# Performance work log

Hardware: AMD Instinct MI355X
Metric: run time of the kernel (lower is better)

Reference implementation:

```python
import jax, jax.numpy as jnp
import numpy as np

B = 4096
D = 1024
N = 9000000
TEMPERATURE = 0.1
GAMMA = 0.8
ALPHA = 0.5
EPS = 1e-14


def setup_inputs() -> dict:
    key = jax.random.key(0)
    k1, k2, k3, k4, k5 = jax.random.split(key, 5)
    zis = jax.random.normal(k1, (B, D), dtype=jnp.float32)
    zjs = jax.random.normal(k2, (B, D), dtype=jnp.float32)
    s_I = jax.random.uniform(k3, (N,), dtype=jnp.float32)
    s_T = jax.random.uniform(k4, (N,), dtype=jnp.float32)
    b_I = jnp.zeros((N,), dtype=jnp.float32)
    b_T = jnp.zeros((N,), dtype=jnp.float32)
    ids = jax.random.randint(k5, (B,), 0, N, dtype=jnp.int64 if jax.config.jax_enable_x64 else jnp.int32)
    return {"zis": zis, "zjs": zjs, "s_I": s_I, "s_T": s_T, "b_I": b_I, "b_T": b_T, "ids": ids}


def reference(zis, zjs, s_I, s_T, b_I, b_T, ids):
    sg = jax.lax.stop_gradient
    # L2 normalize embeddings (norm=True path)
    zis = zis / jnp.linalg.norm(zis, axis=1, keepdims=True)
    zjs = zjs / jnp.linalg.norm(zjs, axis=1, keepdims=True)
    sim = jnp.einsum('id,jd->ij', zis, zjs)            # [B, B]
    diag = jnp.diagonal(sim)                            # [B]
    image_diffs = sim - diag[:, None]
    text_diffs = sim - diag[None, :]
    # detached, temperature-scaled diffs (torch .clone().detach_())
    idd = sg(image_diffs) / TEMPERATURE
    tdd = sg(text_diffs) / TEMPERATURE
    # online max tracking (per-id running max b)
    old_b_I = b_I[ids]                                  # gather [B]
    new_b_I = jnp.maximum(idd.max(axis=1), old_b_I)
    old_b_T = b_T[ids]
    new_b_T = jnp.maximum(tdd.max(axis=0), old_b_T)
    mask_neg = 1.0 - jnp.eye(B, dtype=sim.dtype)
    exp_image_diffs = jnp.exp(idd - new_b_I[:, None]) * mask_neg
    exp_text_diffs = jnp.exp(tdd - new_b_T[None, :]) * mask_neg
    g_I = exp_image_diffs.sum(axis=1) / (B - 1)         # [B]
    g_T = exp_text_diffs.sum(axis=0) / (B - 1)          # [B]
    # EMA of softmax denominator with rescaling for new max
    s_I_new = (1.0 - GAMMA) * s_I[ids] * jnp.exp(old_b_I - new_b_I) + GAMMA * g_I
    s_T_new = (1.0 - GAMMA) * s_T[ids] * jnp.exp(old_b_T - new_b_T) + GAMMA * g_T
    # state writes (side effects in torch; computed for fidelity)
    b_I = b_I.at[ids].set(new_b_I)
    b_T = b_T.at[ids].set(new_b_T)
    s_I = s_I.at[ids].set(s_I_new)
    s_T = s_T.at[ids].set(s_T_new)
    s_I_c = jnp.maximum(s_I_new, EPS)
    s_T_c = jnp.maximum(s_T_new, EPS)
    weights_image = exp_image_diffs / s_I_c[:, None]    # detached weights
    weights_text = exp_text_diffs / s_T_c[None, :]
    image_loss = (weights_image * image_diffs).sum(axis=1) / (B - 1)
    text_loss = (weights_text * text_diffs).sum(axis=0) / (B - 1)
    total_loss = ALPHA * image_loss.mean() + (1.0 - ALPHA) * text_loss.mean()
    return total_loss
```

## Files before the change

### kernel.cpp

```cpp
#include <hip/hip_runtime.h>
#include <stdint.h>

#define B_ 4096
#define D_ 1024
#define TINV 10.0f
#define LOG2E 1.4426950408889634f
#define KE (TINV * LOG2E)
#define INV_BM1 (1.0f / 4095.0f)

typedef __bf16 bf16x8 __attribute__((ext_vector_type(8)));
typedef float f32x4 __attribute__((ext_vector_type(4)));

__device__ __forceinline__ unsigned short f2bf(float x) {
  uint32_t b = __float_as_uint(x);
  b += 0x7FFF + ((b >> 16) & 1);
  return (unsigned short)(b >> 16);
}
__device__ __forceinline__ float bf2f(unsigned short u) {
  return __uint_as_float(((uint32_t)u) << 16);
}

__device__ __forceinline__ void gload16(const void* g, void* l) {
  __builtin_amdgcn_global_load_lds(
      (const __attribute__((address_space(1))) uint32_t*)g,
      (__attribute__((address_space(3))) uint32_t*)l, 16, 0, 0);
}

__global__ __launch_bounds__(256) void k_normalize(const float* __restrict__ zis,
                                                   const float* __restrict__ zjs,
                                                   unsigned short* __restrict__ Abf,
                                                   unsigned short* __restrict__ Bbf) {
  int r = blockIdx.x;
  const float* src;
  unsigned short* dst;
  if (r < B_) { src = zis + (size_t)r * D_; dst = Abf + (size_t)r * D_; }
  else        { src = zjs + (size_t)(r - B_) * D_; dst = Bbf + (size_t)(r - B_) * D_; }
  int t = threadIdx.x;
  float4 v = reinterpret_cast<const float4*>(src)[t];
  float ss = v.x*v.x + v.y*v.y + v.z*v.z + v.w*v.w;
  #pragma unroll
  for (int o = 32; o >= 1; o >>= 1) ss += __shfl_down(ss, o);
  __shared__ float red[4];
  if ((t & 63) == 0) red[t >> 6] = ss;
  __syncthreads();
  float sc = rsqrtf(red[0] + red[1] + red[2] + red[3]);
  ushort4 o4;
  o4.x = f2bf(v.x * sc); o4.y = f2bf(v.y * sc);
  o4.z = f2bf(v.z * sc); o4.w = f2bf(v.w * sc);
  reinterpret_cast<ushort4*>(dst)[t] = o4;
}

__global__ __launch_bounds__(256) void k_gemm(const unsigned short* __restrict__ A,
                                              const unsigned short* __restrict__ B,
                                              unsigned short* __restrict__ C) {
  __shared__ unsigned short As[128 * 32];
  __shared__ unsigned short Bs[128 * 32];
  const int tid = threadIdx.x;
  const int wid = tid >> 6;
  const int lane = tid & 63;
  const int wr = wid >> 1, wc = wid & 1;
  const int by = blockIdx.y, bx = blockIdx.x;

  f32x4 acc[4][4] = {};

  const int lrow = lane >> 2;
  const int lcol = (lane & 3) * 8;
  const int frow = lane & 15;
  const int fcol = (lane >> 4) * 8;

  for (int k0 = 0; k0 < D_; k0 += 32) {
    #pragma unroll
    for (int i = 0; i < 2; ++i) {
      int chunk = i * 4 + wid;
      int r = chunk * 16 + lrow;
      gload16(A + (size_t)(by * 128 + r) * D_ + k0 + lcol, &As[chunk * 512]);
      gload16(B + (size_t)(bx * 128 + r) * D_ + k0 + lcol, &Bs[chunk * 512]);
    }
    __syncthreads();
    bf16x8 af[4], bfr[4];
    #pragma unroll
    for (int m = 0; m < 4; ++m)
      af[m] = *reinterpret_cast<const bf16x8*>(&As[(wr*64 + m*16 + frow) * 32 + fcol]);
    #pragma unroll
    for (int n = 0; n < 4; ++n)
      bfr[n] = *reinterpret_cast<const bf16x8*>(&Bs[(wc*64 + n*16 + frow) * 32 + fcol]);
    #pragma unroll
    for (int m = 0; m < 4; ++m)
      #pragma unroll
      for (int n = 0; n < 4; ++n)
        acc[m][n] = __builtin_amdgcn_mfma_f32_16x16x32_bf16(af[m], bfr[n], acc[m][n], 0, 0, 0);
    __syncthreads();
  }

  const int crow0 = by * 128 + wr * 64;
  const int ccol0 = bx * 128 + wc * 64;
  #pragma unroll
  for (int m = 0; m < 4; ++m)
    #pragma unroll
    for (int n = 0; n < 4; ++n)
      #pragma unroll
      for (int q = 0; q < 4; ++q) {
        int rr = crow0 + m*16 + (lane >> 4)*4 + q;
        int cc = ccol0 + n*16 + (lane & 15);
        C[(size_t)rr * B_ + cc] = f2bf(acc[m][n][q]);
      }
}

__global__ __launch_bounds__(256) void k_fused(const unsigned short* __restrict__ sim,
    const float* __restrict__ bI, const float* __restrict__ sI,
    const int* __restrict__ ids,
    float* __restrict__ LI, float* __restrict__ cmax_p,
    float* __restrict__ cE_p, float* __restrict__ cE2_p) {
  const int i0 = blockIdx.x * 16;
  const int t = threadIdx.x;
  const int w = t >> 6, lane = t & 63;
  __shared__ float rowPart[16][4][3];

  float cmax[16], cE[16], cE2[16];
  #pragma unroll
  for (int k = 0; k < 16; ++k) { cmax[k] = -3.4e38f; cE[k] = 0.f; cE2[k] = 0.f; }

  for (int r = 0; r < 16; ++r) {
    const unsigned short* sp = sim + (size_t)(i0 + r) * B_ + t * 16;
    uint4 u0 = *reinterpret_cast<const uint4*>(sp);
    uint4 u1 = *reinterpret_cast<const uint4*>(sp + 8);
    float x[16];
    x[0]  = __uint_as_float(u0.x << 16); x[1]  = __uint_as_float(u0.x & 0xffff0000u);
    x[2]  = __uint_as_float(u0.y << 16); x[3]  = __uint_as_float(u0.y & 0xffff0000u);
    x[4]  = __uint_as_float(u0.z << 16); x[5]  = __uint_as_float(u0.z & 0xffff0000u);
    x[6]  = __uint_as_float(u0.w << 16); x[7]  = __uint_as_float(u0.w & 0xffff0000u);
    x[8]  = __uint_as_float(u1.x << 16); x[9]  = __uint_as_float(u1.x & 0xffff0000u);
    x[10] = __uint_as_float(u1.y << 16); x[11] = __uint_as_float(u1.y & 0xffff0000u);
    x[12] = __uint_as_float(u1.z << 16); x[13] = __uint_as_float(u1.z & 0xffff0000u);
    x[14] = __uint_as_float(u1.w << 16); x[15] = __uint_as_float(u1.w & 0xffff0000u);
    float rmx = -3.4e38f, rE = 0.f, rE2 = 0.f;
    #pragma unroll
    for (int k = 0; k < 16; ++k) {
      float e = exp2f(x[k] * KE);
      rmx = fmaxf(rmx, x[k]);
      rE += e;
      rE2 = fmaf(e, x[k], rE2);
      cmax[k] = fmaxf(cmax[k], x[k]);
      cE[k] += e;
      cE2[k] = fmaf(e, x[k], cE2[k]);
    }
    #pragma unroll
    for (int o = 32; o >= 1; o >>= 1) {
      rmx = fmaxf(rmx, __shfl_down(rmx, o));
      rE += __shfl_down(rE, o);
      rE2 += __shfl_down(rE2, o);
    }
    if (lane == 0) { rowPart[r][w][0] = rmx; rowPart[r][w][1] = rE; rowPart[r][w][2] = rE2; }
  }
  __syncthreads();
  if (t < 16) {
    int i = i0 + t;
    float mx = fmaxf(fmaxf(rowPart[t][0][0], rowPart[t][1][0]),
                     fmaxf(rowPart[t][2][0], rowPart[t][3][0]));
    float E  = (rowPart[t][0][1] + rowPart[t][1][1]) + (rowPart[t][2][1] + rowPart[t][3][1]);
    float E2 = (rowPart[t][0][2] + rowPart[t][1][2]) + (rowPart[t][2][2] + rowPart[t][3][2]);
    float dg = bf2f(sim[(size_t)i * (B_ + 1)]);
    float ed = exp2f(dg * KE);
    int id = ids[i];
    float oldb = bI[id];
    float newb = fmaxf((mx - dg) * TINV, oldb);
    float sc = exp2f(-(dg * TINV + newb) * LOG2E);
    float S1 = (E - ed) * sc;
    float S2 = (E2 - dg * E) * sc;
    float g = S1 * INV_BM1;
    float sn = 0.2f * sI[id] * exp2f((oldb - newb) * LOG2E) + 0.8f * g;
    LI[i] = S2 / fmaxf(sn, 1e-14f) * INV_BM1;
  }
  size_t base = (size_t)blockIdx.x * B_ + t * 16;
  #pragma unroll
  for (int k = 0; k < 16; ++k) {
    cmax_p[base + k] = cmax[k];
    cE_p[base + k]   = cE[k];
    cE2_p[base + k]  = cE2[k];
  }
}

__global__ __launch_bounds__(256) void k_colred(const unsigned short* __restrict__ sim,
    const float* __restrict__ cmax_p, const float* __restrict__ cE_p,
    const float* __restrict__ cE2_p,
    const float* __restrict__ bT, const float* __restrict__ sT,
    const int* __restrict__ ids, const float* __restrict__ LI,
    float* __restrict__ partial) {
  const int t = threadIdx.x;
  const int cidx = t >> 5;
  const int sub = t & 31;
  const int j = blockIdx.x * 8 + cidx;
  float mx = -3.4e38f, E = 0.f, E2 = 0.f;
  #pragma unroll
  for (int k = 0; k < 8; ++k) {
    size_t o = (size_t)(sub + 32 * k) * B_ + j;
    mx = fmaxf(mx, cmax_p[o]);
    E += cE_p[o];
    E2 += cE2_p[o];
  }
  #pragma unroll
  for (int o = 16; o >= 1; o >>= 1) {
    mx = fmaxf(mx, __shfl_down(mx, o, 32));
    E += __shfl_down(E, o, 32);
    E2 += __shfl_down(E2, o, 32);
  }
  __shared__ float red[8];
  if (sub == 0) {
    float dg = bf2f(sim[(size_t)j * (B_ + 1)]);
    float ed = exp2f(dg * KE);
    int id = ids[j];
    float oldb = bT[id];
    float newb = fmaxf((mx - dg) * TINV, oldb);
    float sc = exp2f(-(dg * TINV + newb) * LOG2E);
    float S1 = (E - ed) * sc;
    float S2 = (E2 - dg * E) * sc;
    float g = S1 * INV_BM1;
    float sn = 0.2f * sT[id] * exp2f((oldb - newb) * LOG2E) + 0.8f * g;
    float lt = S2 / fmaxf(sn, 1e-14f) * INV_BM1;
    red[cidx] = (0.5f * LI[j] + 0.5f * lt) * (1.0f / (float)B_);
  }
  __syncthreads();
  if (t == 0) {
    float s = 0.f;
    #pragma unroll
    for (int k = 0; k < 8; ++k) s += red[k];
    partial[blockIdx.x] = s;
  }
}

__global__ void k_final2(const float* __restrict__ partial, float* __restrict__ out) {
  int t = threadIdx.x;
  float v = partial[t];
  #pragma unroll
  for (int o = 32; o >= 1; o >>= 1) v += __shfl_down(v, o);
  __shared__ float red[8];
  if ((t & 63) == 0) red[t >> 6] = v;
  __syncthreads();
  if (t == 0) {
    float s = 0.f;
    #pragma unroll
    for (int k = 0; k < 8; ++k) s += red[k];
    out[0] = s;
  }
}

extern "C" void kernel_launch(void* const* d_in, const int* in_sizes, int n_in,
                              void* d_out, int out_size, void* d_ws, size_t ws_size,
                              hipStream_t stream) {
  const float* zis = (const float*)d_in[0];
  const float* zjs = (const float*)d_in[1];
  const float* s_I = (const float*)d_in[2];
  const float* s_T = (const float*)d_in[3];
  const float* b_I = (const float*)d_in[4];
  const float* b_T = (const float*)d_in[5];
  const int*   ids = (const int*)d_in[6];

  char* ws = (char*)d_ws;
  size_t off = 0;
  auto alloc = [&](size_t bytes) -> void* {
    void* p = ws + off;
    off = (off + bytes + 255) & ~(size_t)255;
    return p;
  };
  unsigned short* Abf = (unsigned short*)alloc((size_t)B_ * D_ * 2);
  unsigned short* Bbf = (unsigned short*)alloc((size_t)B_ * D_ * 2);
  unsigned short* sim = (unsigned short*)alloc((size_t)B_ * B_ * 2);
  float* cmax_p = (float*)alloc((size_t)256 * B_ * 4);
  float* cE_p   = (float*)alloc((size_t)256 * B_ * 4);
  float* cE2_p  = (float*)alloc((size_t)256 * B_ * 4);
  float* LI     = (float*)alloc(B_ * 4);
  float* partial = (float*)alloc(512 * 4);

  k_normalize<<<2 * B_, 256, 0, stream>>>(zis, zjs, Abf, Bbf);
  k_gemm<<<dim3(32, 32), 256, 0, stream>>>(Abf, Bbf, sim);
  k_fused<<<256, 256, 0, stream>>>(sim, b_I, s_I, ids, LI, cmax_p, cE_p, cE2_p);
  k_colred<<<512, 256, 0, stream>>>(sim, cmax_p, cE_p, cE2_p, b_T, s_T, ids, LI, partial);
  k_final2<<<1, 512, 0, stream>>>(partial, (float*)d_out);
}
```

Baseline: 98.50 us.

## Rewrite GEMM with 256x256 tiles, double-buffered swizzled LDS, and interleaved MFMA/load schedule

Replaces the simple 128x128 bf16 GEMM with a 512-thread kernel using 256x256 output tiles, K=64 steps, double-buffered LDS with XOR swizzle, and a hand-scheduled ping-pong of global-to-LDS loads interleaved with MFMA quadrants, using s_setprio and explicit waitcnts. The goal is to hide memory latency, reduce LDS bank conflicts, and raise MFMA utilization. The epilogue also writes the fp32 diagonal into a separate buffer and packs bf16 pairs into 32-bit stores, so downstream kernels read the diagonal directly. The cost is higher register and LDS pressure and only 256 blocks, which may leave some CUs underused.

Result: faster. 91.36 us (-7.2%).

```diff
diff --git a/kernel.cpp b/kernel.cpp
--- a/kernel.cpp
+++ b/kernel.cpp
@@ -3,6 +3,7 @@
 
 #define B_ 4096
 #define D_ 1024
+#define NT 16
 #define TINV 10.0f
 #define LOG2E 1.4426950408889634f
 #define KE (TINV * LOG2E)
@@ -50,63 +51,134 @@
   reinterpret_cast<ushort4*>(dst)[t] = o4;
 }
 
-__global__ __launch_bounds__(256) void k_gemm(const unsigned short* __restrict__ A,
-                                              const unsigned short* __restrict__ B,
-                                              unsigned short* __restrict__ C) {
-  __shared__ unsigned short As[128 * 32];
-  __shared__ unsigned short Bs[128 * 32];
+#define LDA(MH)                                                              \
+  { _Pragma("unroll") for (int m4_ = 0; m4_ < 4; ++m4_) {                    \
+      const unsigned short* p_ = &Abase[((MH)*64 + m4_*16 + fr) * 64];       \
+      a[m4_][0] = *reinterpret_cast<const bf16x8*>(&p_[ce0]);                \
+      a[m4_][1] = *reinterpret_cast<const bf16x8*>(&p_[ce1]); } }
+
+#define LDB(NH)                                                              \
+  { _Pragma("unroll") for (int n2_ = 0; n2_ < 2; ++n2_) {                    \
+      const unsigned short* p_ = &Bbase[(bn_off + ((NH)*2+n2_)*16 + fr) * 64]; \
+      b[(NH)*2+n2_][0] = *reinterpret_cast<const bf16x8*>(&p_[ce0]);         \
+      b[(NH)*2+n2_][1] = *reinterpret_cast<const bf16x8*>(&p_[ce1]); } }
+
+#define MFMAQ(MH, NH)                                                        \
+  { _Pragma("unroll") for (int m4_ = 0; m4_ < 4; ++m4_) {                    \
+      _Pragma("unroll") for (int n2_ = 0; n2_ < 2; ++n2_) {                  \
+        acc[(MH)*4+m4_][(NH)*2+n2_] = __builtin_amdgcn_mfma_f32_16x16x32_bf16( \
+            a[m4_][0], b[(NH)*2+n2_][0], acc[(MH)*4+m4_][(NH)*2+n2_], 0,0,0);  \
+        acc[(MH)*4+m4_][(NH)*2+n2_] = __builtin_amdgcn_mfma_f32_16x16x32_bf16( \
+            a[m4_][1], b[(NH)*2+n2_][1], acc[(MH)*4+m4_][(NH)*2+n2_], 0,0,0); } } }
+
+#define STAGE_A(T, H)                                                        \
+  { const unsigned short* g_ = Ag + (size_t)((H)*128)*D_ + (T)*64;           \
+    gload16(g_ + so0, &lds[(T)&1][0][H][q0*512]);                            \
+    gload16(g_ + so1, &lds[(T)&1][0][H][q1*512]); }
+
+#define STAGE_B(T, H)                                                        \
+  { const unsigned short* g_ = Bg + (size_t)((H)*128)*D_ + (T)*64;           \
+    gload16(g_ + so0, &lds[(T)&1][1][H][q0*512]);                            \
+    gload16(g_ + so1, &lds[(T)&1][1][H][q1*512]); }
+
+#define SYNC_PRE                                                             \
+  __builtin_amdgcn_s_barrier();                                              \
+  asm volatile("s_waitcnt lgkmcnt(0)" ::: "memory");                         \
+  __builtin_amdgcn_sched_barrier(0);                                         \
+  __builtin_amdgcn_s_setprio(1);
+
+#define SYNC_POST                                                            \
+  __builtin_amdgcn_s_setprio(0);                                             \
+  __builtin_amdgcn_sched_barrier(0);                                         \
+  __builtin_amdgcn_s_barrier();
+
+__global__ __launch_bounds__(512, 2) void k_gemm(const unsigned short* __restrict__ A,
+                                                 const unsigned short* __restrict__ B,
+                                                 unsigned short* __restrict__ C,
+                                                 float* __restrict__ diagp) {
+  __shared__ unsigned short lds[2][2][2][8192];
   const int tid = threadIdx.x;
   const int wid = tid >> 6;
   const int lane = tid & 63;
-  const int wr = wid >> 1, wc = wid & 1;
-  const int by = blockIdx.y, bx = blockIdx.x;
-
-  f32x4 acc[4][4] = {};
-
-  const int lrow = lane >> 2;
-  const int lcol = (lane & 3) * 8;
-  const int frow = lane & 15;
-  const int fcol = (lane >> 4) * 8;
-
-  for (int k0 = 0; k0 < D_; k0 += 32) {
-    #pragma unroll
-    for (int i = 0; i < 2; ++i) {
-      int chunk = i * 4 + wid;
-      int r = chunk * 16 + lrow;
-      gload16(A + (size_t)(by * 128 + r) * D_ + k0 + lcol, &As[chunk * 512]);
-      gload16(B + (size_t)(bx * 128 + r) * D_ + k0 + lcol, &Bs[chunk * 512]);
+  const int wm = wid >> 2;
+  const int wn = wid & 3;
+  const int bRow = blockIdx.y * 256;
+  const int bCol = blockIdx.x * 256;
+  const unsigned short* Ag = A + (size_t)bRow * D_;
+  const unsigned short* Bg = B + (size_t)bCol * D_;
+
+  const int q0 = wid * 2, q1 = q0 + 1;
+  const int srow = q0 * 8 + (lane >> 3);
+  const int scol = ((lane & 7) * 8) ^ (((lane >> 5) & 1) << 4);
+  const size_t so0 = (size_t)srow * D_ + scol;
+  const size_t so1 = (size_t)(srow + 8) * D_ + (scol ^ 32);
+
+  const int fr = lane & 15;
+  const int sx = (((lane >> 2) & 1) << 4) | (((lane >> 3) & 1) << 5);
+  const int ce0 = ((lane >> 4) * 8) ^ sx;
+  const int ce1 = (((lane >> 4) * 8) + 32) ^ sx;
+  const int bn_off = (wn & 1) * 64;
+
+  f32x4 acc[8][4] = {};
+
+  STAGE_A(0, 0); STAGE_A(0, 1); STAGE_B(0, 0); STAGE_B(0, 1);
+  STAGE_B(1, 0); STAGE_A(1, 0);
+  asm volatile("s_waitcnt vmcnt(4)" ::: "memory");
+  __builtin_amdgcn_sched_barrier(0);
+  __builtin_amdgcn_s_barrier();
+
+  for (int t = 0; t < NT; ++t) {
+    const int s = t & 1;
+    const unsigned short* Abase = &lds[s][0][wm][0];
+    const unsigned short* Bbase = &lds[s][1][wn >> 1][0];
+    bf16x8 a[4][2], b[4][2];
+
+    LDA(0); LDB(0);
+    if (t + 1 < NT) { STAGE_B(t + 1, 1); }
+    SYNC_PRE; MFMAQ(0, 0); SYNC_POST;
+
+    LDB(1);
+    if (t + 1 < NT) { STAGE_A(t + 1, 1); }
+    SYNC_PRE; MFMAQ(0, 1); SYNC_POST;
+
+    LDA(1);
+    if (t + 2 < NT) { __builtin_amdgcn_sched_barrier(0); STAGE_B(t + 2, 0); }
+    SYNC_PRE; MFMAQ(1, 0); SYNC_POST;
+
+    if (t + 2 < NT) { __builtin_amdgcn_sched_barrier(0); STAGE_A(t + 2, 0); }
+    __builtin_amdgcn_s_setprio(1);
+    MFMAQ(1, 1);
+    __builtin_amdgcn_s_setprio(0);
+    if (t < NT - 2) {
+      asm volatile("s_waitcnt vmcnt(4)" ::: "memory");
+    } else if (t == NT - 2) {
+      asm volatile("s_waitcnt vmcnt(0)" ::: "memory");
     }
-    __syncthreads();
-    bf16x8 af[4], bfr[4];
-    #pragma unroll
-    for (int m = 0; m < 4; ++m)
-      af[m] = *reinterpret_cast<const bf16x8*>(&As[(wr*64 + m*16 + frow) * 32 + fcol]);
-    #pragma unroll
-    for (int n = 0; n < 4; ++n)
-      bfr[n] = *reinterpret_cast<const bf16x8*>(&Bs[(wc*64 + n*16 + frow) * 32 + fcol]);
-    #pragma unroll
-    for (int m = 0; m < 4; ++m)
-      #pragma unroll
-      for (int n = 0; n < 4; ++n)
-        acc[m][n] = __builtin_amdgcn_mfma_f32_16x16x32_bf16(af[m], bfr[n], acc[m][n], 0, 0, 0);
-    __syncthreads();
-  }
-
-  const int crow0 = by * 128 + wr * 64;
-  const int ccol0 = bx * 128 + wc * 64;
-  #pragma unroll
-  for (int m = 0; m < 4; ++m)
+    __builtin_amdgcn_sched_barrier(0);
+    if (t < NT - 1) __builtin_amdgcn_s_barrier();
+  }
+
+  const int fr4 = (lane >> 4) * 4;
+  #pragma unroll
+  for (int m = 0; m < 8; ++m)
     #pragma unroll
     for (int n = 0; n < 4; ++n)
       #pragma unroll
       for (int q = 0; q < 4; ++q) {
-        int rr = crow0 + m*16 + (lane >> 4)*4 + q;
-        int cc = ccol0 + n*16 + (lane & 15);
-        C[(size_t)rr * B_ + cc] = f2bf(acc[m][n][q]);
+        float v = acc[m][n][q];
+        int rg = bRow + wm * 128 + m * 16 + fr4 + q;
+        int cg = bCol + wn * 64 + n * 16 + fr;
+        if (rg == cg) diagp[rg] = v;
+        float p = __shfl_xor(v, 1);
+        if (!(lane & 1)) {
+          uint32_t u = (uint32_t)f2bf(v) | ((uint32_t)f2bf(p) << 16);
+          *reinterpret_cast<uint32_t*>(&C[(size_t)rg * B_ + cg]) = u;
+        }
       }
 }
 
 __global__ __launch_bounds__(256) void k_fused(const unsigned short* __restrict__ sim,
+    const float* __restrict__ diag,
     const float* __restrict__ bI, const float* __restrict__ sI,
     const int* __restrict__ ids,
     float* __restrict__ LI, float* __restrict__ cmax_p,
@@ -159,7 +231,7 @@
                      fmaxf(rowPart[t][2][0], rowPart[t][3][0]));
     float E  = (rowPart[t][0][1] + rowPart[t][1][1]) + (rowPart[t][2][1] + rowPart[t][3][1]);
     float E2 = (rowPart[t][0][2] + rowPart[t][1][2]) + (rowPart[t][2][2] + rowPart[t][3][2]);
-    float dg = bf2f(sim[(size_t)i * (B_ + 1)]);
+    float dg = diag[i];
     float ed = exp2f(dg * KE);
     int id = ids[i];
     float oldb = bI[id];
@@ -180,7 +252,8 @@
   }
 }
 
-__global__ __launch_bounds__(256) void k_colred(const unsigned short* __restrict__ sim,
+__global__ __launch_bounds__(256) void k_colred(
+    const float* __restrict__ diag,
     const float* __restrict__ cmax_p, const float* __restrict__ cE_p,
     const float* __restrict__ cE2_p,
     const float* __restrict__ bT, const float* __restrict__ sT,
@@ -206,7 +279,7 @@
   }
   __shared__ float red[8];
   if (sub == 0) {
-    float dg = bf2f(sim[(size_t)j * (B_ + 1)]);
+    float dg = diag[j];
     float ed = exp2f(dg * KE);
     int id = ids[j];
     float oldb = bT[id];
@@ -265,6 +338,7 @@
   unsigned short* Abf = (unsigned short*)alloc((size_t)B_ * D_ * 2);
   unsigned short* Bbf = (unsigned short*)alloc((size_t)B_ * D_ * 2);
   unsigned short* sim = (unsigned short*)alloc((size_t)B_ * B_ * 2);
+  float* diag   = (float*)alloc(B_ * 4);
   float* cmax_p = (float*)alloc((size_t)256 * B_ * 4);
   float* cE_p   = (float*)alloc((size_t)256 * B_ * 4);
   float* cE2_p  = (float*)alloc((size_t)256 * B_ * 4);
@@ -272,8 +346,8 @@
   float* partial = (float*)alloc(512 * 4);
 
   k_normalize<<<2 * B_, 256, 0, stream>>>(zis, zjs, Abf, Bbf);
-  k_gemm<<<dim3(32, 32), 256, 0, stream>>>(Abf, Bbf, sim);
-  k_fused<<<256, 256, 0, stream>>>(sim, b_I, s_I, ids, LI, cmax_p, cE_p, cE2_p);
-  k_colred<<<512, 256, 0, stream>>>(sim, cmax_p, cE_p, cE2_p, b_T, s_T, ids, LI, partial);
+  k_gemm<<<dim3(16, 16), 512, 0, stream>>>(Abf, Bbf, sim, diag);
+  k_fused<<<256, 256, 0, stream>>>(sim, diag, b_I, s_I, ids, LI, cmax_p, cE_p, cE2_p);
+  k_colred<<<512, 256, 0, stream>>>(diag, cmax_p, cE_p, cE2_p, b_T, s_T, ids, LI, partial);
   k_final2<<<1, 512, 0, stream>>>(partial, (float*)d_out);
 }
```

## Double-buffer GEMM with 256x128 tiles, swizzled LDS, and fp32 diagonal export

Applied to the files above, without the earlier changes.

Rewrites the similarity GEMM to use 512-thread blocks with 256x128 tiles, a two-stage LDS double buffer with async global-to-LDS loads, XOR-swizzled LDS layout to reduce bank conflicts, and explicit waitcnt/barrier scheduling with raised priority around the MFMA block. The epilogue packs pairs of bf16 outputs into 32-bit stores and writes the fp32 diagonal into a separate buffer, which the row and column reduction kernels now read instead of the bf16 diagonal from sim. The aim is to overlap memory loads with MFMA work and cut per-k-step sync stalls in the dominant GEMM. In exchange it adds a small buffer and more complex hand-tuned synchronisation. The diagonal also changes precision, from a rounded bf16 value to the fp32 value.

Measured after the change: 91.78 us. -6.8%, faster.

```diff
diff --git a/kernel.cpp b/kernel.cpp
--- a/kernel.cpp
+++ b/kernel.cpp
@@ -3,6 +3,10 @@
 
 #define B_ 4096
 #define D_ 1024
+#define BM 256
+#define BN 128
+#define BK 32
+#define NT 32
 #define TINV 10.0f
 #define LOG2E 1.4426950408889634f
 #define KE (TINV * LOG2E)
@@ -50,63 +54,102 @@
   reinterpret_cast<ushort4*>(dst)[t] = o4;
 }
 
-__global__ __launch_bounds__(256) void k_gemm(const unsigned short* __restrict__ A,
-                                              const unsigned short* __restrict__ B,
-                                              unsigned short* __restrict__ C) {
-  __shared__ unsigned short As[128 * 32];
-  __shared__ unsigned short Bs[128 * 32];
+__global__ __launch_bounds__(512, 4) void k_gemm(const unsigned short* __restrict__ A,
+                                                 const unsigned short* __restrict__ B,
+                                                 unsigned short* __restrict__ C,
+                                                 float* __restrict__ diagp) {
+  __shared__ unsigned short lds[2][12288];
   const int tid = threadIdx.x;
   const int wid = tid >> 6;
   const int lane = tid & 63;
-  const int wr = wid >> 1, wc = wid & 1;
-  const int by = blockIdx.y, bx = blockIdx.x;
+  const int wm = wid >> 1;
+  const int wn = wid & 1;
+  const int bRow = blockIdx.y * BM;
+  const int bCol = blockIdx.x * BN;
+  const unsigned short* Ag = A + (size_t)bRow * D_;
+  const unsigned short* Bg = B + (size_t)bCol * D_;
+
+  const int srowA = wid * 32 + (lane >> 2);
+  const int srowB = wid * 16 + (lane >> 2);
+  const int scb   = (((lane & 3) ^ ((lane >> 3) & 3))) * 8;
+  const size_t soA0 = (size_t)srowA * D_ + scb;
+  const size_t soA1 = (size_t)(srowA + 16) * D_ + scb;
+  const size_t soB  = (size_t)srowB * D_ + scb;
+
+  const int fr = lane & 15;
+  const int kq = lane >> 4;
+  const int ce = ((kq ^ ((fr >> 1) & 3)) * 8);
 
   f32x4 acc[4][4] = {};
 
-  const int lrow = lane >> 2;
-  const int lcol = (lane & 3) * 8;
-  const int frow = lane & 15;
-  const int fcol = (lane >> 4) * 8;
-
-  for (int k0 = 0; k0 < D_; k0 += 32) {
-    #pragma unroll
-    for (int i = 0; i < 2; ++i) {
-      int chunk = i * 4 + wid;
-      int r = chunk * 16 + lrow;
-      gload16(A + (size_t)(by * 128 + r) * D_ + k0 + lcol, &As[chunk * 512]);
-      gload16(B + (size_t)(bx * 128 + r) * D_ + k0 + lcol, &Bs[chunk * 512]);
-    }
-    __syncthreads();
-    bf16x8 af[4], bfr[4];
+#define STAGE(T) { const int sl_ = (T) & 1;                                   \
+    const unsigned short* gA_ = Ag + (size_t)(T) * BK;                        \
+    const unsigned short* gB_ = Bg + (size_t)(T) * BK;                        \
+    gload16(gA_ + soA0, &lds[sl_][wid * 1024]);                               \
+    gload16(gA_ + soA1, &lds[sl_][wid * 1024 + 512]);                         \
+    gload16(gB_ + soB,  &lds[sl_][8192 + wid * 512]); }
+
+  STAGE(0); STAGE(1);
+  asm volatile("s_waitcnt vmcnt(3)" ::: "memory");
+  __builtin_amdgcn_sched_barrier(0);
+  __builtin_amdgcn_s_barrier();
+  __builtin_amdgcn_sched_barrier(0);
+
+  for (int t = 0; t < NT; ++t) {
+    const unsigned short* Lb = lds[t & 1];
+    bf16x8 a[4], b[4];
     #pragma unroll
     for (int m = 0; m < 4; ++m)
-      af[m] = *reinterpret_cast<const bf16x8*>(&As[(wr*64 + m*16 + frow) * 32 + fcol]);
+      a[m] = *reinterpret_cast<const bf16x8*>(&Lb[(wm*64 + m*16 + fr) * 32 + ce]);
     #pragma unroll
     for (int n = 0; n < 4; ++n)
-      bfr[n] = *reinterpret_cast<const bf16x8*>(&Bs[(wc*64 + n*16 + frow) * 32 + fcol]);
+      b[n] = *reinterpret_cast<const bf16x8*>(&Lb[8192 + (wn*64 + n*16 + fr) * 32 + ce]);
+    asm volatile("s_waitcnt lgkmcnt(0)" ::: "memory");
+    __builtin_amdgcn_sched_barrier(0);
+    __builtin_amdgcn_s_barrier();
+    __builtin_amdgcn_sched_barrier(0);
+    if (t + 2 < NT) STAGE(t + 2);
+    __builtin_amdgcn_s_setprio(1);
     #pragma unroll
     for (int m = 0; m < 4; ++m)
       #pragma unroll
       for (int n = 0; n < 4; ++n)
-        acc[m][n] = __builtin_amdgcn_mfma_f32_16x16x32_bf16(af[m], bfr[n], acc[m][n], 0, 0, 0);
-    __syncthreads();
-  }
-
-  const int crow0 = by * 128 + wr * 64;
-  const int ccol0 = bx * 128 + wc * 64;
+        acc[m][n] = __builtin_amdgcn_mfma_f32_16x16x32_bf16(a[m], b[n], acc[m][n], 0, 0, 0);
+    __builtin_amdgcn_s_setprio(0);
+    if (t < NT - 2) {
+      asm volatile("s_waitcnt vmcnt(3)" ::: "memory");
+    } else if (t == NT - 2) {
+      asm volatile("s_waitcnt vmcnt(0)" ::: "memory");
+    }
+    __builtin_amdgcn_sched_barrier(0);
+    if (t < NT - 1) {
+      __builtin_amdgcn_s_barrier();
+      __builtin_amdgcn_sched_barrier(0);
+    }
+  }
+
+  const int fr4 = kq * 4;
   #pragma unroll
   for (int m = 0; m < 4; ++m)
     #pragma unroll
     for (int n = 0; n < 4; ++n)
       #pragma unroll
       for (int q = 0; q < 4; ++q) {
-        int rr = crow0 + m*16 + (lane >> 4)*4 + q;
-        int cc = ccol0 + n*16 + (lane & 15);
-        C[(size_t)rr * B_ + cc] = f2bf(acc[m][n][q]);
+        float v = acc[m][n][q];
+        int rg = bRow + wm * 64 + m * 16 + fr4 + q;
+        int cg = bCol + wn * 64 + n * 16 + fr;
+        if (rg == cg) diagp[rg] = v;
+        float p = __shfl_xor(v, 1);
+        if (!(lane & 1)) {
+          uint32_t u = (uint32_t)f2bf(v) | ((uint32_t)f2bf(p) << 16);
+          *reinterpret_cast<uint32_t*>(&C[(size_t)rg * B_ + cg]) = u;
+        }
       }
+#undef STAGE
 }
 
 __global__ __launch_bounds__(256) void k_fused(const unsigned short* __restrict__ sim,
+    const float* __restrict__ diag,
     const float* __restrict__ bI, const float* __restrict__ sI,
     const int* __restrict__ ids,
     float* __restrict__ LI, float* __restrict__ cmax_p,
@@ -159,7 +202,7 @@
                      fmaxf(rowPart[t][2][0], rowPart[t][3][0]));
     float E  = (rowPart[t][0][1] + rowPart[t][1][1]) + (rowPart[t][2][1] + rowPart[t][3][1]);
     float E2 = (rowPart[t][0][2] + rowPart[t][1][2]) + (rowPart[t][2][2] + rowPart[t][3][2]);
-    float dg = bf2f(sim[(size_t)i * (B_ + 1)]);
+    float dg = diag[i];
     float ed = exp2f(dg * KE);
     int id = ids[i];
     float oldb = bI[id];
@@ -180,7 +223,8 @@
   }
 }
 
-__global__ __launch_bounds__(256) void k_colred(const unsigned short* __restrict__ sim,
+__global__ __launch_bounds__(256) void k_colred(
+    const float* __restrict__ diag,
     const float* __restrict__ cmax_p, const float* __restrict__ cE_p,
     const float* __restrict__ cE2_p,
     const float* __restrict__ bT, const float* __restrict__ sT,
@@ -206,7 +250,7 @@
   }
   __shared__ float red[8];
   if (sub == 0) {
-    float dg = bf2f(sim[(size_t)j * (B_ + 1)]);
+    float dg = diag[j];
     float ed = exp2f(dg * KE);
     int id = ids[j];
     float oldb = bT[id];
@@ -265,6 +309,7 @@
   unsigned short* Abf = (unsigned short*)alloc((size_t)B_ * D_ * 2);
   unsigned short* Bbf = (unsigned short*)alloc((size_t)B_ * D_ * 2);
   unsigned short* sim = (unsigned short*)alloc((size_t)B_ * B_ * 2);
+  float* diag   = (float*)alloc(B_ * 4);
   float* cmax_p = (float*)alloc((size_t)256 * B_ * 4);
   float* cE_p   = (float*)alloc((size_t)256 * B_ * 4);
   float* cE2_p  = (float*)alloc((size_t)256 * B_ * 4);
@@ -272,8 +317,8 @@
   float* partial = (float*)alloc(512 * 4);
 
   k_normalize<<<2 * B_, 256, 0, stream>>>(zis, zjs, Abf, Bbf);
-  k_gemm<<<dim3(32, 32), 256, 0, stream>>>(Abf, Bbf, sim);
-  k_fused<<<256, 256, 0, stream>>>(sim, b_I, s_I, ids, LI, cmax_p, cE_p, cE2_p);
-  k_colred<<<512, 256, 0, stream>>>(sim, cmax_p, cE_p, cE2_p, b_T, s_T, ids, LI, partial);
+  k_gemm<<<dim3(B_ / BN, B_ / BM), 512, 0, stream>>>(Abf, Bbf, sim, diag);
+  k_fused<<<256, 256, 0, stream>>>(sim, diag, b_I, s_I, ids, LI, cmax_p, cE_p, cE2_p);
+  k_colred<<<512, 256, 0, stream>>>(diag, cmax_p, cE_p, cE2_p, b_T, s_T, ids, LI, partial);
   k_final2<<<1, 512, 0, stream>>>(partial, (float*)d_out);
 }
```
